# Kernel tuning notes

Measured on AMD Instinct MI355X. Metric: run time of the kernel, lower is better.

Reference implementation:

```python
import jax, jax.numpy as jnp
import numpy as np

EPS = 1e-06  # used both as eps and as the F.threshold threshold (mqjs passes eps as th)


def _pair_log_dist_sum(x1, x2, th):
    # dist[i,j] = ||x1_i||^2 + ||x2_j||^2 - 2 x1_i . x2_j  (n x n)
    x1x2 = x1 @ x2.T
    sq1 = jnp.sum(x1 * x1, axis=1)[:, None]
    sq2 = jnp.sum(x2 * x2, axis=1)[None, :]
    dist = sq1 + sq2 - 2.0 * x1x2
    # F.threshold(dist, th, 1): values <= th -> 1; then clamp(min=1), sqrt, log, row-sum
    dist = jnp.where(dist > th, dist, 1.0)
    dist = jnp.maximum(dist, 1.0)
    return jnp.sum(0.5 * jnp.log(dist), axis=1)  # log(sqrt(d)) == 0.5*log(d)


def _mqjs(inp, tgt, eps):
    n = inp.shape[0]
    x1 = inp.reshape(n, -1)
    x2 = tgt.reshape(n, -1)
    p = (x1 + x2) / 2.0
    ce = _pair_log_dist_sum(x1, p, eps) + _pair_log_dist_sum(x2, p, eps)
    se = _pair_log_dist_sum(x1, x1, eps) * (n / (n - 1))
    return jnp.mean(ce - se)


def setup_inputs() -> dict:
    key = jax.random.key(0)
    k1, k2 = jax.random.split(key)
    n, d = 8192, 256
    inp = jax.random.normal(k1, (n, d), dtype=jnp.float32)
    tgt = jax.random.normal(k2, (n, d), dtype=jnp.float32)
    return {"input": inp, "target": tgt}


def reference(input, target):
    return _mqjs(input, target, EPS)
```

## Files before the change

### kernel.cpp

```cpp
#include <hip/hip_runtime.h>

#define N 8192
#define D 256
#define BM 128
#define BJ 64
#define JG 8
#define GJ (N / BJ / JG)
#define GI (N / BM)
#define NPART (3 * GI * GJ)

typedef int   i32x4 __attribute__((ext_vector_type(4)));
typedef int   i32x8 __attribute__((ext_vector_type(8)));
typedef float f32x4 __attribute__((ext_vector_type(4)));
typedef float f32x2 __attribute__((ext_vector_type(2)));

__device__ __forceinline__ unsigned pack_fp8x4(float a, float b, float c, float d) {
    unsigned lo = __builtin_amdgcn_cvt_pk_fp8_f32(a, b, 0, false);
    return __builtin_amdgcn_cvt_pk_fp8_f32(c, d, lo, true);
}
__device__ __forceinline__ float dequant_sumsq(unsigned q) {
    const float v0 = __builtin_amdgcn_cvt_f32_fp8(q, 0);
    const float v1 = __builtin_amdgcn_cvt_f32_fp8(q, 1);
    const float v2 = __builtin_amdgcn_cvt_f32_fp8(q, 2);
    const float v3 = __builtin_amdgcn_cvt_f32_fp8(q, 3);
    return fmaf(v0, v0, fmaf(v1, v1, fmaf(v2, v2, v3 * v3)));
}

__global__ void prep_kernel(const float* __restrict__ x1, const float* __restrict__ x2,
                            unsigned* __restrict__ x1q, unsigned* __restrict__ x2q,
                            unsigned* __restrict__ pq,
                            float* __restrict__ sq1, float* __restrict__ sq2,
                            float* __restrict__ sqp) {
    const int tid = threadIdx.x, lane = tid & 63, wv = tid >> 6;
    const int row = blockIdx.x * 4 + wv;
    const size_t eb = (size_t)row * D + lane * 4;
    const float4 a = *(const float4*)(x1 + eb);
    const float4 b = *(const float4*)(x2 + eb);
    const float px = 0.5f * (a.x + b.x), py = 0.5f * (a.y + b.y);
    const float pz = 0.5f * (a.z + b.z), pw = 0.5f * (a.w + b.w);
    const unsigned qa = pack_fp8x4(a.x, a.y, a.z, a.w);
    const unsigned qb = pack_fp8x4(b.x, b.y, b.z, b.w);
    const unsigned qp = pack_fp8x4(px, py, pz, pw);
    const size_t wb = (size_t)row * (D / 4) + lane;
    x1q[wb] = qa; x2q[wb] = qb; pq[wb] = qp;
    float s1 = dequant_sumsq(qa), s2 = dequant_sumsq(qb), sp = dequant_sumsq(qp);
    #pragma unroll
    for (int o = 32; o > 0; o >>= 1) {
        s1 += __shfl_down(s1, o, 64);
        s2 += __shfl_down(s2, o, 64);
        sp += __shfl_down(sp, o, 64);
    }
    if (lane == 0) { sq1[row] = s1; sq2[row] = s2; sqp[row] = sp; }
}

__device__ __forceinline__ f32x4 mfma8(i32x8 a, i32x8 b, f32x4 c) {
    return __builtin_amdgcn_mfma_scale_f32_16x16x128_f8f6f4(
        a, b, c, 0, 0, 0, 0x7F7F7F7F, 0, 0x7F7F7F7F);
}

__device__ __forceinline__ i32x8 read_frag(const unsigned char* Ts, int m, int quad) {
    const int r7 = m & 7;
    const i32x4 lo = *(const i32x4*)(Ts + m * 128 + ((((2 * quad)     ^ r7)) << 4));
    const i32x4 hi = *(const i32x4*)(Ts + m * 128 + ((((2 * quad + 1) ^ r7)) << 4));
    i32x8 f;
    f[0] = lo[0]; f[1] = lo[1]; f[2] = lo[2]; f[3] = lo[3];
    f[4] = hi[0]; f[5] = hi[1]; f[6] = hi[2]; f[7] = hi[3];
    return f;
}

__device__ __forceinline__ void stageB(const unsigned char* __restrict__ g,
                                       unsigned char* s, int rowbase, size_t kb,
                                       int wv, int srow, int sblk) {
    #pragma unroll
    for (int it = 0; it < 2; ++it) {
        const int grp = wv * 2 + it;
        const int row = grp * 8 + srow;
        __builtin_amdgcn_global_load_lds(
            (const __attribute__((address_space(1))) void*)(g + (size_t)(rowbase + row) * D + kb + sblk * 16),
            (__attribute__((address_space(3))) void*)(s + grp * 1024), 16, 0, 0);
    }
}

__device__ __forceinline__ float logsumP(const f32x4 (&acc)[4][2],
                                         const f32x2 (&sa01)[4], const f32x2 (&sa23)[4],
                                         const float sb[2]) {
    float s = 0.0f;
    #pragma unroll
    for (int ti = 0; ti < 4; ++ti) {
        f32x2 pr = {1.0f, 1.0f};
        #pragma unroll
        for (int tj = 0; tj < 2; ++tj) {
            const f32x2 sbv = {sb[tj], sb[tj]};
            const f32x2 t01 = sa01[ti] + sbv, t23 = sa23[ti] + sbv;
            const f32x2 v01 = {acc[ti][tj][0], acc[ti][tj][1]};
            const f32x2 v23 = {acc[ti][tj][2], acc[ti][tj][3]};
            f32x2 d01 = t01 - 2.0f * v01;
            f32x2 d23 = t23 - 2.0f * v23;
            d01 = __builtin_elementwise_max(d01, (f32x2){1.0f, 1.0f});
            d23 = __builtin_elementwise_max(d23, (f32x2){1.0f, 1.0f});
            pr *= d01; pr *= d23;
        }
        s += __logf(pr.x * pr.y);
    }
    return s;
}

__device__ __forceinline__ float logsumStraddle(const f32x4 (&acc)[4][2],
                                                const f32x2 (&sa01)[4], const f32x2 (&sa23)[4],
                                                const float sb[2],
                                                int wr, int wc, int quad, int l15,
                                                int I0, int J0) {
    float s = 0.0f;
    #pragma unroll
    for (int ti = 0; ti < 4; ++ti) {
        #pragma unroll
        for (int tj = 0; tj < 2; ++tj) {
            const int j = J0 + wc * 32 + tj * 16 + l15;
            float pr = 1.0f;
            #pragma unroll
            for (int r = 0; r < 4; ++r) {
                const int i = I0 + wr * 64 + ti * 16 + quad * 4 + r;
                const float sav = (r < 2) ? ((r & 1) ? sa01[ti].y : sa01[ti].x)
                                          : ((r & 1) ? sa23[ti].y : sa23[ti].x);
                float d = fmaf(-2.0f, acc[ti][tj][r], sav + sb[tj]);
                d = fmaxf(d, 1.0f);
                const float t = (j > i) ? d : 1.0f;
                const float u = (j >= i) ? d : 1.0f;
                pr *= t * u;
            }
            s += __logf(pr);
        }
    }
    return s;
}

__global__ __launch_bounds__(256) void mqjs_main(
    const unsigned char* __restrict__ x1q, const unsigned char* __restrict__ x2q,
    const unsigned char* __restrict__ pq,
    const float* __restrict__ sq1, const float* __restrict__ sq2,
    const float* __restrict__ sqp, float* __restrict__ partials) {

    __shared__ __align__(16) unsigned char Bs[2][2 * BJ * 128];
    __shared__ float red[4];

    const int tid = threadIdx.x;
    const int lane = tid & 63;
    const int wv = tid >> 6;
    const int wr = wv >> 1, wc = wv & 1;
    const int quad = lane >> 4, l15 = lane & 15;
    const int srow = lane >> 3;
    const int sblk = (lane & 7) ^ srow;

    const int z = blockIdx.z;
    const int I0 = blockIdx.y * BM;
    const int jbase = blockIdx.x * JG;
    const int pid = (z * GI + blockIdx.y) * GJ + blockIdx.x;
    const float wse = -(float)N / (float)(N - 1);

    int jj0 = 0;
    if (z == 2) {
        jj0 = 2 * (int)blockIdx.y - jbase;
        if (jj0 < 0) jj0 = 0;
        if (jj0 >= JG) { if (tid == 0) partials[pid] = 0.0f; return; }
    }

    const unsigned char* Ag = (z == 1) ? x2q : x1q;
    const unsigned char* Bg = (z == 2) ? x1q : pq;
    const float* sqAg = (z == 1) ? sq2 : sq1;
    const float* sqBg = (z == 2) ? sq1 : sqp;

    i32x8 af[2][4];
    f32x2 sa01[4], sa23[4];
    #pragma unroll
    for (int ti = 0; ti < 4; ++ti) {
        #pragma unroll
        for (int kc = 0; kc < 2; ++kc) {
            const size_t ro = (size_t)(I0 + wr * 64 + ti * 16 + l15) * D + kc * 128 + quad * 32;
            af[kc][ti] = *(const i32x8*)(Ag + ro);
        }
        const int sbase = I0 + wr * 64 + ti * 16 + quad * 4;
        sa01[ti] = (f32x2){sqAg[sbase], sqAg[sbase + 1]};
        sa23[ti] = (f32x2){sqAg[sbase + 2], sqAg[sbase + 3]};
    }

    stageB(Bg, Bs[0],        (jbase + jj0) * BJ, 0,   wv, srow, sblk);
    stageB(Bg, Bs[0] + 8192, (jbase + jj0) * BJ, 128, wv, srow, sblk);
    __syncthreads();

    float tsum = 0.0f;

    for (int jj = jj0; jj < JG; ++jj) {
        const int J0 = (jbase + jj) * BJ;
        const int buf = (jj - jj0) & 1;

        float sb[2];
        #pragma unroll
        for (int tj = 0; tj < 2; ++tj) sb[tj] = sqBg[J0 + wc * 32 + tj * 16 + l15];

        f32x4 acc[4][2];
        #pragma unroll
        for (int a = 0; a < 4; ++a)
            #pragma unroll
            for (int b = 0; b < 2; ++b)
                acc[a][b] = (f32x4){0.f, 0.f, 0.f, 0.f};
        #pragma unroll
        for (int kc = 0; kc < 2; ++kc) {
            i32x8 bfr[2];
            #pragma unroll
            for (int tj = 0; tj < 2; ++tj)
                bfr[tj] = read_frag(Bs[buf] + kc * 8192, wc * 32 + tj * 16 + l15, quad);
            #pragma unroll
            for (int ti = 0; ti < 4; ++ti)
                #pragma unroll
                for (int tj = 0; tj < 2; ++tj)
                    acc[ti][tj] = mfma8(af[kc][ti], bfr[tj], acc[ti][tj]);
        }

        if (jj < JG - 1) {
            stageB(Bg, Bs[buf ^ 1],        (jbase + jj + 1) * BJ, 0,   wv, srow, sblk);
            stageB(Bg, Bs[buf ^ 1] + 8192, (jbase + jj + 1) * BJ, 128, wv, srow, sblk);
        }

        if (z < 2) {
            tsum += 0.5f * logsumP(acc, sa01, sa23, sb);
        } else if (J0 >= I0 + BM) {
            tsum += wse * logsumP(acc, sa01, sa23, sb);
        } else {
            tsum += 0.5f * wse * logsumStraddle(acc, sa01, sa23, sb, wr, wc, quad, l15, I0, J0);
        }

        if (jj < JG - 1) __syncthreads();
    }

    #pragma unroll
    for (int o = 32; o > 0; o >>= 1) tsum += __shfl_down(tsum, o, 64);
    if (lane == 0) red[wv] = tsum;
    __syncthreads();
    if (tid == 0) partials[pid] = red[0] + red[1] + red[2] + red[3];
}

__global__ void finalize_kernel(const float* __restrict__ partials, float* __restrict__ out) {
    const int tid = threadIdx.x;
    const float4 v = ((const float4*)partials)[tid];
    double s = (double)v.x + (double)v.y + (double)v.z + (double)v.w;
    #pragma unroll
    for (int o = 32; o > 0; o >>= 1) s += __shfl_down(s, o, 64);
    __shared__ double r[12];
    if ((tid & 63) == 0) r[tid >> 6] = s;
    __syncthreads();
    if (tid == 0) {
        double t = 0.0;
        #pragma unroll
        for (int i = 0; i < 12; ++i) t += r[i];
        out[0] = (float)(t / (double)N);
    }
}

extern "C" void kernel_launch(void* const* d_in, const int* in_sizes, int n_in,
                              void* d_out, int out_size, void* d_ws, size_t ws_size,
                              hipStream_t stream) {
    const float* x1 = (const float*)d_in[0];
    const float* x2 = (const float*)d_in[1];

    char* ws = (char*)d_ws;
    const size_t MBYTES = (size_t)N * D;
    unsigned* x1q = (unsigned*)(ws);
    unsigned* x2q = (unsigned*)(ws + MBYTES);
    unsigned* pq  = (unsigned*)(ws + 2 * MBYTES);
    float* sq1 = (float*)(ws + 3 * MBYTES);
    float* sq2 = (float*)(ws + 3 * MBYTES + (size_t)N * 4);
    float* sqp = (float*)(ws + 3 * MBYTES + (size_t)N * 8);
    float* partials = (float*)(ws + 3 * MBYTES + (size_t)N * 12);

    prep_kernel<<<N / 4, 256, 0, stream>>>(x1, x2, x1q, x2q, pq, sq1, sq2, sqp);
    mqjs_main<<<dim3(GJ, GI, 3), 256, 0, stream>>>(
        (const unsigned char*)x1q, (const unsigned char*)x2q, (const unsigned char*)pq,
        sq1, sq2, sqp, partials);
    finalize_kernel<<<1, 768, 0, stream>>>(partials, (float*)d_out);
}
```

Measured before the change: 143.3 us.

## Load B fragments directly from global into registers, dropping the LDS staging

Removes the shared-memory double buffer and async global-to-LDS staging for the B operand. Each wave now loads its MFMA B fragments straight from global memory into registers, prefetching the next j-tile one iteration ahead, which also removes the per-iteration __syncthreads. The change also swaps __logf for __log2f with a single ln2 rescale at the end, raises MFMA priority around the matmul, and sets launch bounds to two blocks per CU. The cost is redundant global/L2 traffic, since both wave rows now fetch the same B data, plus higher register pressure from holding the prefetched fragments.

```diff
diff --git a/kernel.cpp b/kernel.cpp
--- a/kernel.cpp
+++ b/kernel.cpp
@@ -58,29 +58,6 @@
         a, b, c, 0, 0, 0, 0x7F7F7F7F, 0, 0x7F7F7F7F);
 }
 
-__device__ __forceinline__ i32x8 read_frag(const unsigned char* Ts, int m, int quad) {
-    const int r7 = m & 7;
-    const i32x4 lo = *(const i32x4*)(Ts + m * 128 + ((((2 * quad)     ^ r7)) << 4));
-    const i32x4 hi = *(const i32x4*)(Ts + m * 128 + ((((2 * quad + 1) ^ r7)) << 4));
-    i32x8 f;
-    f[0] = lo[0]; f[1] = lo[1]; f[2] = lo[2]; f[3] = lo[3];
-    f[4] = hi[0]; f[5] = hi[1]; f[6] = hi[2]; f[7] = hi[3];
-    return f;
-}
-
-__device__ __forceinline__ void stageB(const unsigned char* __restrict__ g,
-                                       unsigned char* s, int rowbase, size_t kb,
-                                       int wv, int srow, int sblk) {
-    #pragma unroll
-    for (int it = 0; it < 2; ++it) {
-        const int grp = wv * 2 + it;
-        const int row = grp * 8 + srow;
-        __builtin_amdgcn_global_load_lds(
-            (const __attribute__((address_space(1))) void*)(g + (size_t)(rowbase + row) * D + kb + sblk * 16),
-            (__attribute__((address_space(3))) void*)(s + grp * 1024), 16, 0, 0);
-    }
-}
-
 __device__ __forceinline__ float logsumP(const f32x4 (&acc)[4][2],
                                          const f32x2 (&sa01)[4], const f32x2 (&sa23)[4],
                                          const float sb[2]) {
@@ -100,7 +77,7 @@
             d23 = __builtin_elementwise_max(d23, (f32x2){1.0f, 1.0f});
             pr *= d01; pr *= d23;
         }
-        s += __logf(pr.x * pr.y);
+        s += __log2f(pr.x * pr.y);
     }
     return s;
 }
@@ -128,19 +105,18 @@
                 const float u = (j >= i) ? d : 1.0f;
                 pr *= t * u;
             }
-            s += __logf(pr);
+            s += __log2f(pr);
         }
     }
     return s;
 }
 
-__global__ __launch_bounds__(256) void mqjs_main(
+__global__ __launch_bounds__(256, 2) void mqjs_main(
     const unsigned char* __restrict__ x1q, const unsigned char* __restrict__ x2q,
     const unsigned char* __restrict__ pq,
     const float* __restrict__ sq1, const float* __restrict__ sq2,
     const float* __restrict__ sqp, float* __restrict__ partials) {
 
-    __shared__ __align__(16) unsigned char Bs[2][2 * BJ * 128];
     __shared__ float red[4];
 
     const int tid = threadIdx.x;
@@ -148,8 +124,6 @@
     const int wv = tid >> 6;
     const int wr = wv >> 1, wc = wv & 1;
     const int quad = lane >> 4, l15 = lane & 15;
-    const int srow = lane >> 3;
-    const int sblk = (lane & 7) ^ srow;
 
     const int z = blockIdx.z;
     const int I0 = blockIdx.y * BM;
@@ -183,43 +157,55 @@
         sa23[ti] = (f32x2){sqAg[sbase + 2], sqAg[sbase + 3]};
     }
 
-    stageB(Bg, Bs[0],        (jbase + jj0) * BJ, 0,   wv, srow, sblk);
-    stageB(Bg, Bs[0] + 8192, (jbase + jj0) * BJ, 128, wv, srow, sblk);
-    __syncthreads();
+    const int lb = (wc * 32 + l15) * D + quad * 32;
+    const int sjb = wc * 32 + l15;
+
+    i32x8 c0[2], c1[2];
+    {
+        const unsigned char* bp = Bg + (size_t)(jbase + jj0) * (BJ * D) + lb;
+        #pragma unroll
+        for (int tj = 0; tj < 2; ++tj) {
+            c0[tj] = *(const i32x8*)(bp + tj * (16 * D));
+            c1[tj] = *(const i32x8*)(bp + tj * (16 * D) + 128);
+        }
+    }
+    float sb[2];
+    #pragma unroll
+    for (int tj = 0; tj < 2; ++tj)
+        sb[tj] = sqBg[(jbase + jj0) * BJ + sjb + tj * 16];
 
     float tsum = 0.0f;
+    const f32x4 zero4 = {0.0f, 0.0f, 0.0f, 0.0f};
 
     for (int jj = jj0; jj < JG; ++jj) {
         const int J0 = (jbase + jj) * BJ;
-        const int buf = (jj - jj0) & 1;
-
-        float sb[2];
-        #pragma unroll
-        for (int tj = 0; tj < 2; ++tj) sb[tj] = sqBg[J0 + wc * 32 + tj * 16 + l15];
+        const int jn = (jj + 1 < JG) ? (jj + 1) : (JG - 1);
+
+        i32x8 n0[2], n1[2];
+        const unsigned char* bpn = Bg + (size_t)(jbase + jn) * (BJ * D) + lb;
+        #pragma unroll
+        for (int tj = 0; tj < 2; ++tj) {
+            n0[tj] = *(const i32x8*)(bpn + tj * (16 * D));
+            n1[tj] = *(const i32x8*)(bpn + tj * (16 * D) + 128);
+        }
+        float sbn[2];
+        #pragma unroll
+        for (int tj = 0; tj < 2; ++tj)
+            sbn[tj] = sqBg[(jbase + jn) * BJ + sjb + tj * 16];
 
         f32x4 acc[4][2];
-        #pragma unroll
-        for (int a = 0; a < 4; ++a)
-            #pragma unroll
-            for (int b = 0; b < 2; ++b)
-                acc[a][b] = (f32x4){0.f, 0.f, 0.f, 0.f};
-        #pragma unroll
-        for (int kc = 0; kc < 2; ++kc) {
-            i32x8 bfr[2];
+        __builtin_amdgcn_s_setprio(1);
+        #pragma unroll
+        for (int ti = 0; ti < 4; ++ti)
             #pragma unroll
             for (int tj = 0; tj < 2; ++tj)
-                bfr[tj] = read_frag(Bs[buf] + kc * 8192, wc * 32 + tj * 16 + l15, quad);
+                acc[ti][tj] = mfma8(af[0][ti], c0[tj], zero4);
+        #pragma unroll
+        for (int ti = 0; ti < 4; ++ti)
             #pragma unroll
-            for (int ti = 0; ti < 4; ++ti)
-                #pragma unroll
-                for (int tj = 0; tj < 2; ++tj)
-                    acc[ti][tj] = mfma8(af[kc][ti], bfr[tj], acc[ti][tj]);
-        }
-
-        if (jj < JG - 1) {
-            stageB(Bg, Bs[buf ^ 1],        (jbase + jj + 1) * BJ, 0,   wv, srow, sblk);
-            stageB(Bg, Bs[buf ^ 1] + 8192, (jbase + jj + 1) * BJ, 128, wv, srow, sblk);
-        }
+            for (int tj = 0; tj < 2; ++tj)
+                acc[ti][tj] = mfma8(af[1][ti], c1[tj], acc[ti][tj]);
+        __builtin_amdgcn_s_setprio(0);
 
         if (z < 2) {
             tsum += 0.5f * logsumP(acc, sa01, sa23, sb);
@@ -229,9 +215,12 @@
             tsum += 0.5f * wse * logsumStraddle(acc, sa01, sa23, sb, wr, wc, quad, l15, I0, J0);
         }
 
-        if (jj < JG - 1) __syncthreads();
-    }
-
+        c0[0] = n0[0]; c0[1] = n0[1];
+        c1[0] = n1[0]; c1[1] = n1[1];
+        sb[0] = sbn[0]; sb[1] = sbn[1];
+    }
+
+    tsum *= 0.6931471805599453f;
     #pragma unroll
     for (int o = 32; o > 0; o >>= 1) tsum += __shfl_down(tsum, o, 64);
     if (lane == 0) red[wv] = tsum;
```

Result: slower. 186.8 us (+30.3%).

## Triple-buffer B tiles with prefetch distance two and log2 accumulation

Applied to the files above, without the earlier changes.

Moves B staging from double to triple buffering, prefetching two tiles ahead. A manual vmcnt wait plus s_barrier replaces __syncthreads, so global loads stay in flight across the MFMA and log epilogue. It also hoists all B fragment reads ahead of the MFMA chain, raises wave priority around the MFMAs, and uses log2 with a single ln2 scale at the end instead of natural log. This costs extra LDS, which may lower occupancy, and relies on the exact vmcnt count matching how many loads stageB issues.

```diff
diff --git a/kernel.cpp b/kernel.cpp
--- a/kernel.cpp
+++ b/kernel.cpp
@@ -100,7 +100,7 @@
             d23 = __builtin_elementwise_max(d23, (f32x2){1.0f, 1.0f});
             pr *= d01; pr *= d23;
         }
-        s += __logf(pr.x * pr.y);
+        s += __log2f(pr.x * pr.y);
     }
     return s;
 }
@@ -128,7 +128,7 @@
                 const float u = (j >= i) ? d : 1.0f;
                 pr *= t * u;
             }
-            s += __logf(pr);
+            s += __log2f(pr);
         }
     }
     return s;
@@ -140,7 +140,7 @@
     const float* __restrict__ sq1, const float* __restrict__ sq2,
     const float* __restrict__ sqp, float* __restrict__ partials) {
 
-    __shared__ __align__(16) unsigned char Bs[2][2 * BJ * 128];
+    __shared__ __align__(16) unsigned char Bs[3][2 * BJ * 128];
     __shared__ float red[4];
 
     const int tid = threadIdx.x;
@@ -185,41 +185,52 @@
 
     stageB(Bg, Bs[0],        (jbase + jj0) * BJ, 0,   wv, srow, sblk);
     stageB(Bg, Bs[0] + 8192, (jbase + jj0) * BJ, 128, wv, srow, sblk);
-    __syncthreads();
+    if (jj0 + 1 < JG) {
+        stageB(Bg, Bs[1],        (jbase + jj0 + 1) * BJ, 0,   wv, srow, sblk);
+        stageB(Bg, Bs[1] + 8192, (jbase + jj0 + 1) * BJ, 128, wv, srow, sblk);
+    }
 
     float tsum = 0.0f;
+    const f32x4 zero4 = {0.0f, 0.0f, 0.0f, 0.0f};
+    int cur = 0;
 
     for (int jj = jj0; jj < JG; ++jj) {
         const int J0 = (jbase + jj) * BJ;
-        const int buf = (jj - jj0) & 1;
+
+        if (jj + 1 < JG) asm volatile("s_waitcnt vmcnt(4)" ::: "memory");
+        else             asm volatile("s_waitcnt vmcnt(0)" ::: "memory");
+        asm volatile("s_barrier" ::: "memory");
 
         float sb[2];
         #pragma unroll
         for (int tj = 0; tj < 2; ++tj) sb[tj] = sqBg[J0 + wc * 32 + tj * 16 + l15];
 
+        if (jj + 2 < JG) {
+            const int b2 = (cur == 0) ? 2 : cur - 1;
+            stageB(Bg, Bs[b2],        (jbase + jj + 2) * BJ, 0,   wv, srow, sblk);
+            stageB(Bg, Bs[b2] + 8192, (jbase + jj + 2) * BJ, 128, wv, srow, sblk);
+        }
+
+        i32x8 bfr0[2], bfr1[2];
+        #pragma unroll
+        for (int tj = 0; tj < 2; ++tj) {
+            bfr0[tj] = read_frag(Bs[cur],        wc * 32 + tj * 16 + l15, quad);
+            bfr1[tj] = read_frag(Bs[cur] + 8192, wc * 32 + tj * 16 + l15, quad);
+        }
+
         f32x4 acc[4][2];
-        #pragma unroll
-        for (int a = 0; a < 4; ++a)
-            #pragma unroll
-            for (int b = 0; b < 2; ++b)
-                acc[a][b] = (f32x4){0.f, 0.f, 0.f, 0.f};
-        #pragma unroll
-        for (int kc = 0; kc < 2; ++kc) {
-            i32x8 bfr[2];
+        __builtin_amdgcn_s_setprio(1);
+        #pragma unroll
+        for (int ti = 0; ti < 4; ++ti)
             #pragma unroll
             for (int tj = 0; tj < 2; ++tj)
-                bfr[tj] = read_frag(Bs[buf] + kc * 8192, wc * 32 + tj * 16 + l15, quad);
+                acc[ti][tj] = mfma8(af[0][ti], bfr0[tj], zero4);
+        #pragma unroll
+        for (int ti = 0; ti < 4; ++ti)
             #pragma unroll
-            for (int ti = 0; ti < 4; ++ti)
-                #pragma unroll
-                for (int tj = 0; tj < 2; ++tj)
-                    acc[ti][tj] = mfma8(af[kc][ti], bfr[tj], acc[ti][tj]);
-        }
-
-        if (jj < JG - 1) {
-            stageB(Bg, Bs[buf ^ 1],        (jbase + jj + 1) * BJ, 0,   wv, srow, sblk);
-            stageB(Bg, Bs[buf ^ 1] + 8192, (jbase + jj + 1) * BJ, 128, wv, srow, sblk);
-        }
+            for (int tj = 0; tj < 2; ++tj)
+                acc[ti][tj] = mfma8(af[1][ti], bfr1[tj], acc[ti][tj]);
+        __builtin_amdgcn_s_setprio(0);
 
         if (z < 2) {
             tsum += 0.5f * logsumP(acc, sa01, sa23, sb);
@@ -229,9 +240,10 @@
             tsum += 0.5f * wse * logsumStraddle(acc, sa01, sa23, sb, wr, wc, quad, l15, I0, J0);
         }
 
-        if (jj < JG - 1) __syncthreads();
-    }
-
+        cur = (cur == 2) ? 0 : cur + 1;
+    }
+
+    tsum *= 0.6931471805599453f;
     #pragma unroll
     for (int o = 32; o > 0; o >>= 1) tsum += __shfl_down(tsum, o, 64);
     if (lane == 0) red[wv] = tsum;
```

New measurement: 147.0 us. 1.03x slower.
